# Kernel tuning notes

Hardware: AMD Instinct MI355X
Metric: run time of the kernel (lower is better)

Reference implementation:

```python
import jax, jax.numpy as jnp
import numpy as np

H = 256        # hidden_dim
GD = 16        # genome_dim
GL = 16        # genome_len
L = 2          # n_layers
NH = 4         # n_heads
ED = 256       # embed_dim (of generated network)
CS = 256       # chunk_size (== H so chunk feedback into GRU is well-formed)
TOTAL = 4 * ED * ED + 4 * ED          # 263168
NCH = (TOTAL + CS - 1) // CS          # 1028 sequential GRU steps
B = 16


def setup_inputs() -> dict:
    key = jax.random.key(0)
    ks = iter(jax.random.split(key, 32))
    def p(shape, s=0.02):
        return jax.random.normal(next(ks), shape, jnp.float32) * s
    return dict(
        genome_seq=jax.random.normal(next(ks), (B, GL, GD), jnp.float32),
        embed_W=p((H, GD)), embed_b=jnp.zeros((H,), jnp.float32),
        qkv_W=p((L, 3 * H, H)), qkv_b=jnp.zeros((L, 3 * H), jnp.float32),
        attn_out_W=p((L, H, H)), attn_out_b=jnp.zeros((L, H), jnp.float32),
        ln1_g=jnp.ones((L, H), jnp.float32), ln1_b=jnp.zeros((L, H), jnp.float32),
        ln2_g=jnp.ones((L, H), jnp.float32), ln2_b=jnp.zeros((L, H), jnp.float32),
        ffn_W1=p((L, 4 * H, H)), ffn_b1=jnp.zeros((L, 4 * H), jnp.float32),
        ffn_W2=p((L, H, 4 * H)), ffn_b2=jnp.zeros((L, H), jnp.float32),
        gru_Wih=p((3 * H, H)), gru_Whh=p((3 * H, H)),
        gru_bih=jnp.zeros((3 * H,), jnp.float32), gru_bhh=jnp.zeros((3 * H,), jnp.float32),
        out_W=p((CS, H)), out_b=jnp.zeros((CS,), jnp.float32),
    )


def _ln(x, g, b, eps=1e-5):
    m = x.mean(-1, keepdims=True)
    v = ((x - m) ** 2).mean(-1, keepdims=True)
    return (x - m) / jnp.sqrt(v + eps) * g + b


def reference(genome_seq, embed_W, embed_b, qkv_W, qkv_b, attn_out_W, attn_out_b,
              ln1_g, ln1_b, ln2_g, ln2_b, ffn_W1, ffn_b1, ffn_W2, ffn_b2,
              gru_Wih, gru_Whh, gru_bih, gru_bhh, out_W, out_b):
    b = genome_seq.shape[0]
    dh = H // NH
    scale = 1.0 / np.sqrt(dh).astype(np.float32)

    h = genome_seq @ embed_W.T + embed_b                      # [B, S, H]
    # post-norm transformer encoder, relu FFN (PyTorch defaults, no dropout)
    for l in range(L):
        qkv = h @ qkv_W[l].T + qkv_b[l]                        # [B, S, 3H]
        q, k, v = jnp.split(qkv, 3, axis=-1)
        q = q.reshape(b, GL, NH, dh)
        k = k.reshape(b, GL, NH, dh)
        v = v.reshape(b, GL, NH, dh)
        scores = jnp.einsum('bshd,bthd->bhst', q, k) * scale
        attn = jax.nn.softmax(scores, axis=-1)
        o = jnp.einsum('bhst,bthd->bshd', attn, v).reshape(b, GL, H)
        h = _ln(h + o @ attn_out_W[l].T + attn_out_b[l], ln1_g[l], ln1_b[l])
        f = jax.nn.relu(h @ ffn_W1[l].T + ffn_b1[l]) @ ffn_W2[l].T + ffn_b2[l]
        h = _ln(h + f, ln2_g[l], ln2_b[l])

    latent = h.mean(axis=1)                                    # [B, H]

    # sequential chunk generation: 1 GRU step + Linear per chunk, fed back
    def step(carry, _):
        x, hid = carry
        gi = x @ gru_Wih.T + gru_bih
        gh = hid @ gru_Whh.T + gru_bhh
        ir, iz, inn = jnp.split(gi, 3, axis=-1)
        hr, hz, hn = jnp.split(gh, 3, axis=-1)
        r = jax.nn.sigmoid(ir + hr)
        z = jax.nn.sigmoid(iz + hz)
        n = jnp.tanh(inn + r * hn)
        hid = (1.0 - z) * n + z * hid
        chunk = hid @ out_W.T + out_b                          # [B, CS]
        return (chunk, hid), chunk

    h0 = jnp.zeros((b, H), latent.dtype)
    _, chunks = jax.lax.scan(step, (latent, h0), None, length=NCH)  # [NCH, B, CS]
    flat = jnp.moveaxis(chunks, 0, 1).reshape(b, NCH * CS)
    return flat[:, :TOTAL]
```

## Files before the change

kernel.cpp:

```cpp
#include <hip/hip_runtime.h>


typedef unsigned int uint_t;
typedef int v4i __attribute__((ext_vector_type(4)));

static constexpr size_t WS_HB   = 0;
static constexpr size_t WS_AO   = 262144;
static constexpr size_t WS_GI0  = 593920;
static constexpr size_t WS_CV   = 606208;
static constexpr size_t WS_MS   = 607232;
static constexpr size_t WS_M8   = 608256;
static constexpr size_t WS_HSEQ = 673792;

__device__ inline float sigf(float x){
    return __builtin_amdgcn_rcpf(1.0f + __builtin_amdgcn_exp2f(-1.442695041f*x));
}
__device__ inline float tanh_fast(float x){
    return 1.0f - 2.0f*__builtin_amdgcn_rcpf(1.0f + __builtin_amdgcn_exp2f(2.885390082f*x));
}


__global__ __launch_bounds__(256) void k_emb_prep(
    const float* gs, const float* eW, const float* eb,
    const float* Wih, const float* Whh, const float* bih, const float* bhh,
    const float* outW, const float* outb, float* ws)
{
    __shared__ float wrow[256]; __shared__ float red[256];
    __shared__ signed char q8[256];

    if(blockIdx.x < 256){
        int bs = blockIdx.x;
        int i  = threadIdx.x;
        const float* g = gs + bs*16;
        float acc = eb[i];
#pragma unroll
        for(int d=0; d<16; ++d) acc += g[d]*eW[i*16+d];
        ws[WS_HB + (size_t)bs*256 + i] = acc;
        return;
    }

    int r = blockIdx.x - 256, c = threadIdx.x;
    bool hasA = (r<768);
    wrow[c] = hasA ? Wih[(size_t)r*256+c] : 0.0f;
    __syncthreads();
    float m;
    if(hasA){
        float a=0.f;
        for(int k=0;k<256;++k) a += wrow[k]*outW[(size_t)k*256+c];
        if(r<512) a += Whh[(size_t)r*256+c];
        m=a;
    } else {
        m = Whh[(size_t)(r-256)*256+c];
    }
    red[c] = wrow[c]*outb[c];
    __syncthreads();
    for(int off=128;off>0;off>>=1){ if(c<off) red[c]+=red[c+off]; __syncthreads(); }
    if(c==0){
        float cv;
        if(r<512)       cv = red[0] + bih[r] + bhh[r];
        else if(r<768)  cv = red[0] + bih[r];
        else            cv = bhh[r-256];
        ws[WS_CV + r] = cv;
    }
    __syncthreads();
    red[c] = fabsf(m);
    __syncthreads();
    for(int off=128;off>0;off>>=1){ if(c<off) red[c]=fmaxf(red[c],red[c+off]); __syncthreads(); }
    float rowmax = red[0];
    float inv = rowmax>0.f ? 127.0f/rowmax : 0.0f;
    q8[c] = (signed char)__float2int_rn(m*inv);
    if(c==0) ws[WS_MS + r] = rowmax>0.f ? rowmax*(1.0f/(127.0f*127.0f)) : 0.0f;
    __syncthreads();
    if(c<64){
        uint_t u = ((uint_t)(unsigned char)q8[4*c  ])
                 | ((uint_t)(unsigned char)q8[4*c+1] << 8)
                 | ((uint_t)(unsigned char)q8[4*c+2] << 16)
                 | ((uint_t)(unsigned char)q8[4*c+3] << 24);
        ((uint_t*)ws)[WS_M8 + (size_t)r*64 + c] = u;
    }
}


__global__ __launch_bounds__(256) void k_qkv_attn(const float* qkvW, const float* qkvb,
                                                  float* ws, int l){
    __shared__ float s_h[16][256];
    __shared__ float s_q[16][64], s_k[16][64], s_v[16][64];
    __shared__ float s_sc[16][16];
    int b = blockIdx.x>>2, hh = blockIdx.x&3;
    int tid = threadIdx.x;

    for(int u=tid; u<4096; u+=256)
        s_h[u>>8][u&255] = ws[WS_HB + (size_t)(b*16+(u>>8))*256 + (u&255)];
    __syncthreads();

    if(tid<192){
        int p = tid>>6, d = tid&63;
        int row = l*768 + p*256 + hh*64 + d;
        const float* wr = qkvW + (size_t)row*256;
        float bias = qkvb[row];
        float acc[16];
#pragma unroll
        for(int s=0;s<16;++s) acc[s]=bias;
        for(int k=0;k<256;k+=4){
            float4 w4 = *(const float4*)(wr+k);
#pragma unroll
            for(int s=0;s<16;++s){
                float4 h4 = *(const float4*)&s_h[s][k];
                acc[s] += w4.x*h4.x + w4.y*h4.y + w4.z*h4.z + w4.w*h4.w;
            }
        }
        float (*dst)[64] = (p==0) ? s_q : (p==1) ? s_k : s_v;
#pragma unroll
        for(int s=0;s<16;++s) dst[s][d] = acc[s];
    }
    __syncthreads();

    {
        int s = tid>>4, t = tid&15;
        float a=0.f;
#pragma unroll
        for(int d=0; d<64; ++d) a += s_q[s][d]*s_k[t][d];
        s_sc[s][t] = a*0.125f;
    }
    __syncthreads();
    if(tid<16){
        int r=tid;
        float m=-1e30f;
#pragma unroll
        for(int tt=0;tt<16;++tt) m=fmaxf(m,s_sc[r][tt]);
        float e[16]; float sum=0.f;
#pragma unroll
        for(int tt=0;tt<16;++tt){ e[tt]=__expf(s_sc[r][tt]-m); sum+=e[tt]; }
        float inv=1.0f/sum;
#pragma unroll
        for(int tt=0;tt<16;++tt) s_sc[r][tt]=e[tt]*inv;
    }
    __syncthreads();
    for(int u=tid; u<1024; u+=256){
        int s=u>>6, d=u&63;
        float o=0.f;
#pragma unroll
        for(int t2=0;t2<16;++t2) o += s_sc[s][t2]*s_v[t2][d];
        ws[WS_AO + (size_t)(b*16+s)*256 + hh*64 + d] = o;
    }
}


__global__ __launch_bounds__(256) void k_ao_ffn(
    const float* aoW, const float* aob, const float* g1, const float* b1,
    const float* W1, const float* fb1, const float* W2, const float* fb2,
    const float* g2, const float* b2v, float* ws, int l)
{
    __shared__ float s_x[256];
    __shared__ float s_f1[1024];
    __shared__ float red[256];
    int bs = blockIdx.x, i = threadIdx.x;

    s_x[i] = ws[WS_AO + (size_t)bs*256 + i];
    float hb = ws[WS_HB + (size_t)bs*256 + i];
    __syncthreads();

    const float* wr = aoW + (size_t)(l*256+i)*256;
    float acc = aob[l*256+i];
    for(int k=0;k<256;k+=4){
        float4 w4 = *(const float4*)(wr+k);
        float4 h4 = *(const float4*)&s_x[k];
        acc += w4.x*h4.x + w4.y*h4.y + w4.z*h4.z + w4.w*h4.w;
    }
    float x = hb + acc;
    red[i]=x; __syncthreads();
    for(int off=128;off>0;off>>=1){ if(i<off) red[i]+=red[i+off]; __syncthreads(); }
    float mn = red[0]*(1.0f/256.0f); __syncthreads();
    float d = x-mn;
    red[i]=d*d; __syncthreads();
    for(int off=128;off>0;off>>=1){ if(i<off) red[i]+=red[i+off]; __syncthreads(); }
    float vv = red[0]*(1.0f/256.0f);
    float h1 = (d / sqrtf(vv+1e-5f))*g1[l*256+i] + b1[l*256+i];
    __syncthreads();
    s_x[i] = h1;
    __syncthreads();

#pragma unroll
    for(int jj=0;jj<4;++jj){
        int j = jj*256 + i;
        const float* w1r = W1 + (size_t)(l*1024+j)*256;
        float a1 = fb1[l*1024+j];
        for(int k=0;k<256;k+=4){
            float4 w4 = *(const float4*)(w1r+k);
            float4 h4 = *(const float4*)&s_x[k];
            a1 += w4.x*h4.x + w4.y*h4.y + w4.z*h4.z + w4.w*h4.w;
        }
        s_f1[j] = fmaxf(a1, 0.0f);
    }
    __syncthreads();

    const float* w2r = W2 + (size_t)(l*256+i)*1024;
    float a2 = fb2[l*256+i];
    for(int k=0;k<1024;k+=4){
        float4 w4 = *(const float4*)(w2r+k);
        float4 h4 = *(const float4*)&s_f1[k];
        a2 += w4.x*h4.x + w4.y*h4.y + w4.z*h4.z + w4.w*h4.w;
    }
    float x2 = h1 + a2;
    red[i]=x2; __syncthreads();
    for(int off=128;off>0;off>>=1){ if(i<off) red[i]+=red[i+off]; __syncthreads(); }
    float mn2 = red[0]*(1.0f/256.0f); __syncthreads();
    float d2 = x2-mn2;
    red[i]=d2*d2; __syncthreads();
    for(int off=128;off>0;off>>=1){ if(i<off) red[i]+=red[i+off]; __syncthreads(); }
    float vv2 = red[0]*(1.0f/256.0f);
    float y2 = d2 / sqrtf(vv2+1e-5f);
    ws[WS_HB + (size_t)bs*256 + i] = y2*g2[l*256+i] + b2v[l*256+i];
}


__global__ __launch_bounds__(768) void k_lat_gi0(const float* Wih, const float* bih,
                                                 float* ws){
    __shared__ float lat[256];
    int b=blockIdx.x, j=threadIdx.x;
    if(j<256){
        float a=0.f;
#pragma unroll
        for(int s=0;s<16;++s) a += ws[WS_HB + (size_t)(b*16+s)*256 + j];
        lat[j] = a*(1.0f/16.0f);
    }
    __syncthreads();
    const float* wr = Wih + (size_t)j*256;
    float acc = bih[j];
    for(int k=0;k<256;k+=4){
        float4 w4=*(const float4*)(wr+k);
        float4 l4=*(const float4*)&lat[k];
        acc += w4.x*l4.x + w4.y*l4.y + w4.z*l4.z + w4.w*l4.w;
    }
    ws[WS_GI0 + (size_t)b*768 + j] = acc;
}


__global__ __launch_bounds__(512,2) void k_chain(const float* bhh, float* ws){
    __shared__ alignas(16) signed char h8[2][256];
    int tid = threadIdx.x;
    int b   = blockIdx.x;
    int l   = tid & 63;
    int w   = tid >> 6;
    int col = l & 15;
    int grp = l >> 4;
    int par = grp & 1;
    int ge  = w*32 + par*16 + col;

    const uint_t* Mdw = (const uint_t*)ws + WS_M8;

    v4i wf[8][4];
#pragma unroll
    for(int s=0;s<4;++s){
#pragma unroll
        for(int half=0; half<2; ++half){
            int f = s*2 + half;
            int row = s*256 + w*32 + half*16 + col;
            const uint_t* src = Mdw + (size_t)row*64 + grp*4;
#pragma unroll
            for(int kt=0;kt<4;++kt)
                wf[f][kt] = *(const v4i*)(src + kt*16);
        }
    }
    float Cs[4], MSs[4];
#pragma unroll
    for(int s=0;s<4;++s){
        int row = s*256 + ge;
        Cs[s]  = ws[WS_CV + row];
        MSs[s] = ws[WS_MS + row];
    }

    const float* gi = ws + WS_GI0 + (size_t)b*768;
    float r0 = sigf(gi[ge]     + bhh[ge]);
    float z0 = sigf(gi[256+ge] + bhh[256+ge]);
    float n0 = tanh_fast(gi[512+ge] + r0*bhh[512+ge]);
    float hp = (1.0f-z0)*n0;

    float* hsp = ws + WS_HSEQ + (size_t)b*256;
    if(grp < 2){
        h8[0][w*32 + (l&31)] = (signed char)__float2int_rn(hp*127.0f);
        hsp[w*32 + (l&31)] = hp;
    }
    asm volatile("s_waitcnt lgkmcnt(0)" ::: "memory");
    __builtin_amdgcn_s_barrier();
    asm volatile("" ::: "memory");

    const v4i vzero = {0,0,0,0};
    int po = 0;
    for(int t=1; t<1028; ++t){
        hsp += 4096;
        v4i af[4];
#pragma unroll
        for(int kt=0;kt<4;++kt)
            af[kt] = *(const v4i*)&h8[po][kt*64 + grp*16];
        v4i acc[8];
#pragma unroll
        for(int f=0;f<8;++f){
            acc[f] = __builtin_amdgcn_mfma_i32_16x16x64_i8(af[0], wf[f][0], vzero, 0,0,0);
#pragma unroll
            for(int kt=1;kt<4;++kt)
                acc[f] = __builtin_amdgcn_mfma_i32_16x16x64_i8(af[kt], wf[f][kt], acc[f], 0,0,0);
        }
        int a_r = par ? acc[1][0] : acc[0][0];
        int a_z = par ? acc[3][0] : acc[2][0];
        int a_n = par ? acc[5][0] : acc[4][0];
        int a_h = par ? acc[7][0] : acc[6][0];
        float yr = MSs[0]*(float)a_r + Cs[0];
        float yz = MSs[1]*(float)a_z + Cs[1];
        float yn = MSs[2]*(float)a_n + Cs[2];
        float yh = MSs[3]*(float)a_h + Cs[3];
        float rr = sigf(yr);
        float zz = sigf(yz);
        float nn = tanh_fast(yn + rr*yh);
        hp = (1.0f-zz)*nn + zz*hp;
        if(grp < 2){
            h8[po^1][w*32 + (l&31)] = (signed char)__float2int_rn(hp*127.0f);
            hsp[w*32 + (l&31)] = hp;
        }
        asm volatile("s_waitcnt lgkmcnt(0)" ::: "memory");
        __builtin_amdgcn_s_barrier();
        asm volatile("" ::: "memory");
        po ^= 1;
    }
}

__global__ __launch_bounds__(256) void k_epi(const float* outW, const float* outb,
                                             const float* ws, float* out){
    __shared__ float ht[16][256];
    int t = blockIdx.x, j = threadIdx.x;
    for(int idx=j; idx<4096; idx+=256)
        ht[idx>>8][idx&255] = ws[WS_HSEQ + (size_t)t*4096 + idx];
    __syncthreads();
    const float* wr = outW + (size_t)j*256;
    float bias = outb[j];
    float acc[16];
#pragma unroll
    for(int bb=0;bb<16;++bb) acc[bb]=bias;
    for(int k=0;k<256;k+=4){
        float4 w4 = *(const float4*)(wr+k);
#pragma unroll
        for(int bb=0;bb<16;++bb)
            acc[bb] += w4.x*ht[bb][k]+w4.y*ht[bb][k+1]+w4.z*ht[bb][k+2]+w4.w*ht[bb][k+3];
    }
#pragma unroll
    for(int bb=0;bb<16;++bb)
        out[(size_t)bb*263168 + (size_t)t*256 + j] = acc[bb];
}


extern "C" void kernel_launch(void* const* d_in, const int* in_sizes, int n_in,
                              void* d_out, int out_size, void* d_ws, size_t ws_size,
                              hipStream_t stream){
    const float* gs   = (const float*)d_in[0];
    const float* eW   = (const float*)d_in[1];
    const float* eb   = (const float*)d_in[2];
    const float* qkvW = (const float*)d_in[3];
    const float* qkvb = (const float*)d_in[4];
    const float* aoW  = (const float*)d_in[5];
    const float* aob  = (const float*)d_in[6];
    const float* g1   = (const float*)d_in[7];
    const float* b1   = (const float*)d_in[8];
    const float* g2   = (const float*)d_in[9];
    const float* b2   = (const float*)d_in[10];
    const float* W1   = (const float*)d_in[11];
    const float* fb1  = (const float*)d_in[12];
    const float* W2   = (const float*)d_in[13];
    const float* fb2  = (const float*)d_in[14];
    const float* Wih  = (const float*)d_in[15];
    const float* Whh  = (const float*)d_in[16];
    const float* bih  = (const float*)d_in[17];
    const float* bhh  = (const float*)d_in[18];
    const float* outW = (const float*)d_in[19];
    const float* outb = (const float*)d_in[20];
    float* ws  = (float*)d_ws;
    float* out = (float*)d_out;

    k_emb_prep<<<1280,256,0,stream>>>(gs,eW,eb,Wih,Whh,bih,bhh,outW,outb,ws);
    for(int l=0;l<2;++l){
        k_qkv_attn<<<64,256,0,stream>>>(qkvW,qkvb,ws,l);
        k_ao_ffn  <<<256,256,0,stream>>>(aoW,aob,g1,b1,W1,fb1,W2,fb2,g2,b2,ws,l);
    }
    k_lat_gi0<<<16,768,0,stream>>>(Wih,bih,ws);
    k_chain  <<<16,512,0,stream>>>(bhh,ws);
    k_epi    <<<1028,256,0,stream>>>(outW,outb,ws,out);
}
```

Measured before the change: 1.096 ms.

## Fuse all stages into one cooperative persistent kernel with grid syncs

Replaces the seven separate kernel launches with a single cooperative kernel of 128 blocks that steps through embedding, transformer layers, GRU weight prep, the sequential chain and the epilogue, using grid.sync between stages. The weight-quantization prep now runs on idle blocks in parallel with the layer-0 attention, and its reductions use wave shuffles. This targets launch overhead and inter-kernel gaps. In exchange the epilogue and FFN stages run on only 128 blocks instead of up to 1028, so there is less parallelism and more register pressure from the merged kernel.

```diff
diff --git a/kernel.cpp b/kernel.cpp
--- a/kernel.cpp
+++ b/kernel.cpp
@@ -1,4 +1,7 @@
 #include <hip/hip_runtime.h>
+#include <hip/hip_cooperative_groups.h>
+
+namespace cg = cooperative_groups;
 
 
 typedef unsigned int uint_t;
@@ -19,332 +22,336 @@
     return 1.0f - 2.0f*__builtin_amdgcn_rcpf(1.0f + __builtin_amdgcn_exp2f(2.885390082f*x));
 }
 
-
-__global__ __launch_bounds__(256) void k_emb_prep(
+__global__ __launch_bounds__(512,2) void k_all(
     const float* gs, const float* eW, const float* eb,
-    const float* Wih, const float* Whh, const float* bih, const float* bhh,
-    const float* outW, const float* outb, float* ws)
+    const float* qkvW, const float* qkvb,
+    const float* aoW, const float* aob,
+    const float* g1, const float* b1, const float* g2, const float* b2v,
+    const float* W1, const float* fb1, const float* W2, const float* fb2,
+    const float* Wih, const float* bih, const float* Whh, const float* bhh,
+    const float* outW, const float* outb,
+    float* ws, float* out)
 {
-    __shared__ float wrow[256]; __shared__ float red[256];
-    __shared__ signed char q8[256];
-
-    if(blockIdx.x < 256){
-        int bs = blockIdx.x;
-        int i  = threadIdx.x;
+    __shared__ float s_h[16][256];
+    __shared__ float s_qkv[3][16][64];
+    __shared__ float s_sc[16][16];
+    __shared__ float s_f1[2][1024];
+    __shared__ float s_red[2][256];
+    __shared__ signed char s_h8[2][256];
+
+    cg::grid_group grid = cg::this_grid();
+    int tid = threadIdx.x;
+    int bx  = blockIdx.x;
+
+    {
+        int bs = bx*2 + (tid>>8);
+        int i  = tid & 255;
         const float* g = gs + bs*16;
         float acc = eb[i];
 #pragma unroll
         for(int d=0; d<16; ++d) acc += g[d]*eW[i*16+d];
         ws[WS_HB + (size_t)bs*256 + i] = acc;
-        return;
-    }
-
-    int r = blockIdx.x - 256, c = threadIdx.x;
-    bool hasA = (r<768);
-    wrow[c] = hasA ? Wih[(size_t)r*256+c] : 0.0f;
-    __syncthreads();
-    float m;
-    if(hasA){
-        float a=0.f;
-        for(int k=0;k<256;++k) a += wrow[k]*outW[(size_t)k*256+c];
-        if(r<512) a += Whh[(size_t)r*256+c];
-        m=a;
-    } else {
-        m = Whh[(size_t)(r-256)*256+c];
-    }
-    red[c] = wrow[c]*outb[c];
-    __syncthreads();
-    for(int off=128;off>0;off>>=1){ if(c<off) red[c]+=red[c+off]; __syncthreads(); }
-    if(c==0){
-        float cv;
-        if(r<512)       cv = red[0] + bih[r] + bhh[r];
-        else if(r<768)  cv = red[0] + bih[r];
-        else            cv = bhh[r-256];
-        ws[WS_CV + r] = cv;
-    }
-    __syncthreads();
-    red[c] = fabsf(m);
-    __syncthreads();
-    for(int off=128;off>0;off>>=1){ if(c<off) red[c]=fmaxf(red[c],red[c+off]); __syncthreads(); }
-    float rowmax = red[0];
-    float inv = rowmax>0.f ? 127.0f/rowmax : 0.0f;
-    q8[c] = (signed char)__float2int_rn(m*inv);
-    if(c==0) ws[WS_MS + r] = rowmax>0.f ? rowmax*(1.0f/(127.0f*127.0f)) : 0.0f;
-    __syncthreads();
-    if(c<64){
-        uint_t u = ((uint_t)(unsigned char)q8[4*c  ])
-                 | ((uint_t)(unsigned char)q8[4*c+1] << 8)
-                 | ((uint_t)(unsigned char)q8[4*c+2] << 16)
-                 | ((uint_t)(unsigned char)q8[4*c+3] << 24);
-        ((uint_t*)ws)[WS_M8 + (size_t)r*64 + c] = u;
-    }
-}
-
-
-__global__ __launch_bounds__(256) void k_qkv_attn(const float* qkvW, const float* qkvb,
-                                                  float* ws, int l){
-    __shared__ float s_h[16][256];
-    __shared__ float s_q[16][64], s_k[16][64], s_v[16][64];
-    __shared__ float s_sc[16][16];
-    int b = blockIdx.x>>2, hh = blockIdx.x&3;
-    int tid = threadIdx.x;
-
-    for(int u=tid; u<4096; u+=256)
-        s_h[u>>8][u&255] = ws[WS_HB + (size_t)(b*16+(u>>8))*256 + (u&255)];
-    __syncthreads();
-
-    if(tid<192){
-        int p = tid>>6, d = tid&63;
-        int row = l*768 + p*256 + hh*64 + d;
-        const float* wr = qkvW + (size_t)row*256;
-        float bias = qkvb[row];
-        float acc[16];
-#pragma unroll
-        for(int s=0;s<16;++s) acc[s]=bias;
-        for(int k=0;k<256;k+=4){
-            float4 w4 = *(const float4*)(wr+k);
-#pragma unroll
-            for(int s=0;s<16;++s){
-                float4 h4 = *(const float4*)&s_h[s][k];
-                acc[s] += w4.x*h4.x + w4.y*h4.y + w4.z*h4.z + w4.w*h4.w;
-            }
-        }
-        float (*dst)[64] = (p==0) ? s_q : (p==1) ? s_k : s_v;
-#pragma unroll
-        for(int s=0;s<16;++s) dst[s][d] = acc[s];
-    }
-    __syncthreads();
-
-    {
-        int s = tid>>4, t = tid&15;
-        float a=0.f;
-#pragma unroll
-        for(int d=0; d<64; ++d) a += s_q[s][d]*s_k[t][d];
-        s_sc[s][t] = a*0.125f;
-    }
-    __syncthreads();
-    if(tid<16){
-        int r=tid;
-        float m=-1e30f;
-#pragma unroll
-        for(int tt=0;tt<16;++tt) m=fmaxf(m,s_sc[r][tt]);
-        float e[16]; float sum=0.f;
-#pragma unroll
-        for(int tt=0;tt<16;++tt){ e[tt]=__expf(s_sc[r][tt]-m); sum+=e[tt]; }
-        float inv=1.0f/sum;
-#pragma unroll
-        for(int tt=0;tt<16;++tt) s_sc[r][tt]=e[tt]*inv;
-    }
-    __syncthreads();
-    for(int u=tid; u<1024; u+=256){
-        int s=u>>6, d=u&63;
-        float o=0.f;
-#pragma unroll
-        for(int t2=0;t2<16;++t2) o += s_sc[s][t2]*s_v[t2][d];
-        ws[WS_AO + (size_t)(b*16+s)*256 + hh*64 + d] = o;
-    }
-}
-
-
-__global__ __launch_bounds__(256) void k_ao_ffn(
-    const float* aoW, const float* aob, const float* g1, const float* b1,
-    const float* W1, const float* fb1, const float* W2, const float* fb2,
-    const float* g2, const float* b2v, float* ws, int l)
-{
-    __shared__ float s_x[256];
-    __shared__ float s_f1[1024];
-    __shared__ float red[256];
-    int bs = blockIdx.x, i = threadIdx.x;
-
-    s_x[i] = ws[WS_AO + (size_t)bs*256 + i];
-    float hb = ws[WS_HB + (size_t)bs*256 + i];
-    __syncthreads();
-
-    const float* wr = aoW + (size_t)(l*256+i)*256;
-    float acc = aob[l*256+i];
-    for(int k=0;k<256;k+=4){
-        float4 w4 = *(const float4*)(wr+k);
-        float4 h4 = *(const float4*)&s_x[k];
-        acc += w4.x*h4.x + w4.y*h4.y + w4.z*h4.z + w4.w*h4.w;
-    }
-    float x = hb + acc;
-    red[i]=x; __syncthreads();
-    for(int off=128;off>0;off>>=1){ if(i<off) red[i]+=red[i+off]; __syncthreads(); }
-    float mn = red[0]*(1.0f/256.0f); __syncthreads();
-    float d = x-mn;
-    red[i]=d*d; __syncthreads();
-    for(int off=128;off>0;off>>=1){ if(i<off) red[i]+=red[i+off]; __syncthreads(); }
-    float vv = red[0]*(1.0f/256.0f);
-    float h1 = (d / sqrtf(vv+1e-5f))*g1[l*256+i] + b1[l*256+i];
-    __syncthreads();
-    s_x[i] = h1;
-    __syncthreads();
-
-#pragma unroll
-    for(int jj=0;jj<4;++jj){
-        int j = jj*256 + i;
-        const float* w1r = W1 + (size_t)(l*1024+j)*256;
-        float a1 = fb1[l*1024+j];
-        for(int k=0;k<256;k+=4){
-            float4 w4 = *(const float4*)(w1r+k);
-            float4 h4 = *(const float4*)&s_x[k];
-            a1 += w4.x*h4.x + w4.y*h4.y + w4.z*h4.z + w4.w*h4.w;
-        }
-        s_f1[j] = fmaxf(a1, 0.0f);
-    }
-    __syncthreads();
-
-    const float* w2r = W2 + (size_t)(l*256+i)*1024;
-    float a2 = fb2[l*256+i];
-    for(int k=0;k<1024;k+=4){
-        float4 w4 = *(const float4*)(w2r+k);
-        float4 h4 = *(const float4*)&s_f1[k];
-        a2 += w4.x*h4.x + w4.y*h4.y + w4.z*h4.z + w4.w*h4.w;
-    }
-    float x2 = h1 + a2;
-    red[i]=x2; __syncthreads();
-    for(int off=128;off>0;off>>=1){ if(i<off) red[i]+=red[i+off]; __syncthreads(); }
-    float mn2 = red[0]*(1.0f/256.0f); __syncthreads();
-    float d2 = x2-mn2;
-    red[i]=d2*d2; __syncthreads();
-    for(int off=128;off>0;off>>=1){ if(i<off) red[i]+=red[i+off]; __syncthreads(); }
-    float vv2 = red[0]*(1.0f/256.0f);
-    float y2 = d2 / sqrtf(vv2+1e-5f);
-    ws[WS_HB + (size_t)bs*256 + i] = y2*g2[l*256+i] + b2v[l*256+i];
-}
-
-
-__global__ __launch_bounds__(768) void k_lat_gi0(const float* Wih, const float* bih,
-                                                 float* ws){
-    __shared__ float lat[256];
-    int b=blockIdx.x, j=threadIdx.x;
-    if(j<256){
-        float a=0.f;
-#pragma unroll
-        for(int s=0;s<16;++s) a += ws[WS_HB + (size_t)(b*16+s)*256 + j];
-        lat[j] = a*(1.0f/16.0f);
-    }
-    __syncthreads();
-    const float* wr = Wih + (size_t)j*256;
-    float acc = bih[j];
-    for(int k=0;k<256;k+=4){
-        float4 w4=*(const float4*)(wr+k);
-        float4 l4=*(const float4*)&lat[k];
-        acc += w4.x*l4.x + w4.y*l4.y + w4.z*l4.z + w4.w*l4.w;
-    }
-    ws[WS_GI0 + (size_t)b*768 + j] = acc;
-}
-
-
-__global__ __launch_bounds__(512,2) void k_chain(const float* bhh, float* ws){
-    __shared__ alignas(16) signed char h8[2][256];
-    int tid = threadIdx.x;
-    int b   = blockIdx.x;
-    int l   = tid & 63;
-    int w   = tid >> 6;
-    int col = l & 15;
-    int grp = l >> 4;
-    int par = grp & 1;
-    int ge  = w*32 + par*16 + col;
-
-    const uint_t* Mdw = (const uint_t*)ws + WS_M8;
-
-    v4i wf[8][4];
-#pragma unroll
-    for(int s=0;s<4;++s){
-#pragma unroll
-        for(int half=0; half<2; ++half){
-            int f = s*2 + half;
-            int row = s*256 + w*32 + half*16 + col;
-            const uint_t* src = Mdw + (size_t)row*64 + grp*4;
-#pragma unroll
-            for(int kt=0;kt<4;++kt)
-                wf[f][kt] = *(const v4i*)(src + kt*16);
-        }
-    }
-    float Cs[4], MSs[4];
-#pragma unroll
-    for(int s=0;s<4;++s){
-        int row = s*256 + ge;
-        Cs[s]  = ws[WS_CV + row];
-        MSs[s] = ws[WS_MS + row];
-    }
-
-    const float* gi = ws + WS_GI0 + (size_t)b*768;
-    float r0 = sigf(gi[ge]     + bhh[ge]);
-    float z0 = sigf(gi[256+ge] + bhh[256+ge]);
-    float n0 = tanh_fast(gi[512+ge] + r0*bhh[512+ge]);
-    float hp = (1.0f-z0)*n0;
-
-    float* hsp = ws + WS_HSEQ + (size_t)b*256;
-    if(grp < 2){
-        h8[0][w*32 + (l&31)] = (signed char)__float2int_rn(hp*127.0f);
-        hsp[w*32 + (l&31)] = hp;
-    }
-    asm volatile("s_waitcnt lgkmcnt(0)" ::: "memory");
-    __builtin_amdgcn_s_barrier();
-    asm volatile("" ::: "memory");
-
-    const v4i vzero = {0,0,0,0};
-    int po = 0;
-    for(int t=1; t<1028; ++t){
-        hsp += 4096;
-        v4i af[4];
-#pragma unroll
-        for(int kt=0;kt<4;++kt)
-            af[kt] = *(const v4i*)&h8[po][kt*64 + grp*16];
-        v4i acc[8];
-#pragma unroll
-        for(int f=0;f<8;++f){
-            acc[f] = __builtin_amdgcn_mfma_i32_16x16x64_i8(af[0], wf[f][0], vzero, 0,0,0);
-#pragma unroll
-            for(int kt=1;kt<4;++kt)
-                acc[f] = __builtin_amdgcn_mfma_i32_16x16x64_i8(af[kt], wf[f][kt], acc[f], 0,0,0);
-        }
-        int a_r = par ? acc[1][0] : acc[0][0];
-        int a_z = par ? acc[3][0] : acc[2][0];
-        int a_n = par ? acc[5][0] : acc[4][0];
-        int a_h = par ? acc[7][0] : acc[6][0];
-        float yr = MSs[0]*(float)a_r + Cs[0];
-        float yz = MSs[1]*(float)a_z + Cs[1];
-        float yn = MSs[2]*(float)a_n + Cs[2];
-        float yh = MSs[3]*(float)a_h + Cs[3];
-        float rr = sigf(yr);
-        float zz = sigf(yz);
-        float nn = tanh_fast(yn + rr*yh);
-        hp = (1.0f-zz)*nn + zz*hp;
+    }
+    grid.sync();
+
+    for(int l=0; l<2; ++l){
+        if(bx < 64){
+            int b = bx>>2, hh = bx&3;
+            for(int u=tid; u<4096; u+=512)
+                s_h[u>>8][u&255] = ws[WS_HB + (size_t)(b*16+(u>>8))*256 + (u&255)];
+            __syncthreads();
+            if(tid<192){
+                int p = tid>>6, d = tid&63;
+                int row = l*768 + p*256 + hh*64 + d;
+                const float* wr = qkvW + (size_t)row*256;
+                float bias = qkvb[row];
+                float acc[16];
+#pragma unroll
+                for(int s=0;s<16;++s) acc[s]=bias;
+                for(int k=0;k<256;k+=4){
+                    float4 w4 = *(const float4*)(wr+k);
+#pragma unroll
+                    for(int s=0;s<16;++s){
+                        float4 h4 = *(const float4*)&s_h[s][k];
+                        acc[s] += w4.x*h4.x + w4.y*h4.y + w4.z*h4.z + w4.w*h4.w;
+                    }
+                }
+#pragma unroll
+                for(int s=0;s<16;++s) s_qkv[p][s][d] = acc[s];
+            }
+            __syncthreads();
+            if(tid<256){
+                int s = tid>>4, t = tid&15;
+                float a=0.f;
+#pragma unroll
+                for(int d=0; d<64; ++d) a += s_qkv[0][s][d]*s_qkv[1][t][d];
+                s_sc[s][t] = a*0.125f;
+            }
+            __syncthreads();
+            if(tid<16){
+                int r=tid;
+                float m=-1e30f;
+#pragma unroll
+                for(int tt=0;tt<16;++tt) m=fmaxf(m,s_sc[r][tt]);
+                float e[16]; float sum=0.f;
+#pragma unroll
+                for(int tt=0;tt<16;++tt){ e[tt]=__expf(s_sc[r][tt]-m); sum+=e[tt]; }
+                float inv=1.0f/sum;
+#pragma unroll
+                for(int tt=0;tt<16;++tt) s_sc[r][tt]=e[tt]*inv;
+            }
+            __syncthreads();
+            for(int u=tid; u<1024; u+=512){
+                int s=u>>6, d=u&63;
+                float o=0.f;
+#pragma unroll
+                for(int t2=0;t2<16;++t2) o += s_sc[s][t2]*s_qkv[2][t2][d];
+                ws[WS_AO + (size_t)(b*16+s)*256 + hh*64 + d] = o;
+            }
+        } else if(l==0){
+            int pb = bx - 64;
+            float* wrow = &s_f1[0][0];
+            float* redf = &s_red[0][0];
+            signed char* q8 = (signed char*)&s_sc[0][0];
+            int rh = tid>>8, c = tid&255, wv = tid>>6;
+            for(int it=0; it<8; ++it){
+                int r = pb*16 + it*2 + rh;
+                bool hasA = (r < 768);
+                wrow[rh*256+c] = hasA ? Wih[(size_t)r*256+c] : 0.0f;
+                __syncthreads();
+                float m;
+                if(hasA){
+                    float a = 0.f;
+                    for(int k=0;k<256;++k) a += wrow[rh*256+k]*outW[(size_t)k*256+c];
+                    if(r<512) a += Whh[(size_t)r*256+c];
+                    m = a;
+                } else {
+                    m = Whh[(size_t)(r-256)*256+c];
+                }
+                float pv = wrow[rh*256+c]*outb[c];
+                for(int mk=1; mk<64; mk<<=1) pv += __shfl_xor(pv, mk);
+                if((tid&63)==0) redf[wv] = pv;
+                __syncthreads();
+                if(c==0){
+                    float cs = redf[rh*4+0]+redf[rh*4+1]+redf[rh*4+2]+redf[rh*4+3];
+                    float cv;
+                    if(r<512)       cv = cs + bih[r] + bhh[r];
+                    else if(r<768)  cv = cs + bih[r];
+                    else            cv = bhh[r-256];
+                    ws[WS_CV + r] = cv;
+                }
+                float av = fabsf(m);
+                for(int mk=1; mk<64; mk<<=1) av = fmaxf(av, __shfl_xor(av, mk));
+                if((tid&63)==0) redf[16+wv] = av;
+                __syncthreads();
+                float rowmax = fmaxf(fmaxf(redf[16+rh*4],redf[17+rh*4]),
+                                     fmaxf(redf[18+rh*4],redf[19+rh*4]));
+                float inv = rowmax>0.f ? 127.0f/rowmax : 0.0f;
+                q8[rh*256+c] = (signed char)__float2int_rn(m*inv);
+                if(c==0) ws[WS_MS + r] = rowmax>0.f ? rowmax*(1.0f/(127.0f*127.0f)) : 0.0f;
+                __syncthreads();
+                if(c<64){
+                    uint_t u = ((uint_t)(unsigned char)q8[rh*256+4*c  ])
+                             | ((uint_t)(unsigned char)q8[rh*256+4*c+1] << 8)
+                             | ((uint_t)(unsigned char)q8[rh*256+4*c+2] << 16)
+                             | ((uint_t)(unsigned char)q8[rh*256+4*c+3] << 24);
+                    ((uint_t*)ws)[WS_M8 + (size_t)r*64 + c] = u;
+                }
+                __syncthreads();
+            }
+        }
+        grid.sync();
+
+        {
+            int tk = tid>>8, i = tid&255;
+            int bs = bx*2 + tk;
+            s_h[tk][i] = ws[WS_AO + (size_t)bs*256 + i];
+            float hb = ws[WS_HB + (size_t)bs*256 + i];
+            __syncthreads();
+            const float* wr = aoW + (size_t)(l*256+i)*256;
+            float acc = aob[l*256+i];
+            for(int k=0;k<256;k+=4){
+                float4 w4 = *(const float4*)(wr+k);
+                float4 h4 = *(const float4*)&s_h[tk][k];
+                acc += w4.x*h4.x + w4.y*h4.y + w4.z*h4.z + w4.w*h4.w;
+            }
+            float x = hb + acc;
+            s_red[tk][i]=x; __syncthreads();
+            for(int off=128;off>0;off>>=1){ if(i<off) s_red[tk][i]+=s_red[tk][i+off]; __syncthreads(); }
+            float mn = s_red[tk][0]*(1.0f/256.0f); __syncthreads();
+            float d = x-mn;
+            s_red[tk][i]=d*d; __syncthreads();
+            for(int off=128;off>0;off>>=1){ if(i<off) s_red[tk][i]+=s_red[tk][i+off]; __syncthreads(); }
+            float vv = s_red[tk][0]*(1.0f/256.0f);
+            float h1 = (d / sqrtf(vv+1e-5f))*g1[l*256+i] + b1[l*256+i];
+            __syncthreads();
+            s_h[2+tk][i] = h1;
+            __syncthreads();
+#pragma unroll
+            for(int jj=0;jj<4;++jj){
+                int j = jj*256 + i;
+                const float* w1r = W1 + (size_t)(l*1024+j)*256;
+                float a1 = fb1[l*1024+j];
+                for(int k=0;k<256;k+=4){
+                    float4 w4 = *(const float4*)(w1r+k);
+                    float4 h4 = *(const float4*)&s_h[2+tk][k];
+                    a1 += w4.x*h4.x + w4.y*h4.y + w4.z*h4.z + w4.w*h4.w;
+                }
+                s_f1[tk][j] = fmaxf(a1, 0.0f);
+            }
+            __syncthreads();
+            const float* w2r = W2 + (size_t)(l*256+i)*1024;
+            float a2 = fb2[l*256+i];
+            for(int k=0;k<1024;k+=4){
+                float4 w4 = *(const float4*)(w2r+k);
+                float4 h4 = *(const float4*)&s_f1[tk][k];
+                a2 += w4.x*h4.x + w4.y*h4.y + w4.z*h4.z + w4.w*h4.w;
+            }
+            float x2 = h1 + a2;
+            s_red[tk][i]=x2; __syncthreads();
+            for(int off=128;off>0;off>>=1){ if(i<off) s_red[tk][i]+=s_red[tk][i+off]; __syncthreads(); }
+            float mn2 = s_red[tk][0]*(1.0f/256.0f); __syncthreads();
+            float d2 = x2-mn2;
+            s_red[tk][i]=d2*d2; __syncthreads();
+            for(int off=128;off>0;off>>=1){ if(i<off) s_red[tk][i]+=s_red[tk][i+off]; __syncthreads(); }
+            float vv2 = s_red[tk][0]*(1.0f/256.0f);
+            float y2 = d2 / sqrtf(vv2+1e-5f);
+            ws[WS_HB + (size_t)bs*256 + i] = y2*g2[l*256+i] + b2v[l*256+i];
+        }
+        grid.sync();
+    }
+
+    if(bx < 16){
+        float* lat = &s_sc[0][0];
+        if(tid<256){
+            float a=0.f;
+#pragma unroll
+            for(int s=0;s<16;++s) a += ws[WS_HB + (size_t)(bx*16+s)*256 + tid];
+            lat[tid] = a*(1.0f/16.0f);
+        }
+        __syncthreads();
+        for(int j=tid; j<768; j+=512){
+            const float* wr = Wih + (size_t)j*256;
+            float acc = bih[j];
+            for(int k=0;k<256;k+=4){
+                float4 w4=*(const float4*)(wr+k);
+                float4 l4=*(const float4*)&lat[k];
+                acc += w4.x*l4.x + w4.y*l4.y + w4.z*l4.z + w4.w*l4.w;
+            }
+            ws[WS_GI0 + (size_t)bx*768 + j] = acc;
+        }
+    }
+    grid.sync();
+
+    if(bx < 16){
+        int b   = bx;
+        int ln  = tid & 63;
+        int w   = tid >> 6;
+        int col = ln & 15;
+        int grp = ln >> 4;
+        int par = grp & 1;
+        int ge  = w*32 + par*16 + col;
+
+        const uint_t* Mdw = (const uint_t*)ws + WS_M8;
+        v4i wf[8][4];
+#pragma unroll
+        for(int s=0;s<4;++s){
+#pragma unroll
+            for(int half=0; half<2; ++half){
+                int f = s*2 + half;
+                int row = s*256 + w*32 + half*16 + col;
+                const uint_t* src = Mdw + (size_t)row*64 + grp*4;
+#pragma unroll
+                for(int kt=0;kt<4;++kt)
+                    wf[f][kt] = *(const v4i*)(src + kt*16);
+            }
+        }
+        float Cs[4], MSs[4];
+#pragma unroll
+        for(int s=0;s<4;++s){
+            int row = s*256 + ge;
+            Cs[s]  = ws[WS_CV + row];
+            MSs[s] = ws[WS_MS + row];
+        }
+
+        const float* gi = ws + WS_GI0 + (size_t)b*768;
+        float r0 = sigf(gi[ge]     + bhh[ge]);
+        float z0 = sigf(gi[256+ge] + bhh[256+ge]);
+        float n0 = tanh_fast(gi[512+ge] + r0*bhh[512+ge]);
+        float hp = (1.0f-z0)*n0;
+
+        float* hsp = ws + WS_HSEQ + (size_t)b*256;
         if(grp < 2){
-            h8[po^1][w*32 + (l&31)] = (signed char)__float2int_rn(hp*127.0f);
-            hsp[w*32 + (l&31)] = hp;
+            s_h8[0][w*32 + (ln&31)] = (signed char)__float2int_rn(hp*127.0f);
+            hsp[w*32 + (ln&31)] = hp;
         }
         asm volatile("s_waitcnt lgkmcnt(0)" ::: "memory");
         __builtin_amdgcn_s_barrier();
         asm volatile("" ::: "memory");
-        po ^= 1;
-    }
-}
-
-__global__ __launch_bounds__(256) void k_epi(const float* outW, const float* outb,
-                                             const float* ws, float* out){
-    __shared__ float ht[16][256];
-    int t = blockIdx.x, j = threadIdx.x;
-    for(int idx=j; idx<4096; idx+=256)
-        ht[idx>>8][idx&255] = ws[WS_HSEQ + (size_t)t*4096 + idx];
-    __syncthreads();
-    const float* wr = outW + (size_t)j*256;
-    float bias = outb[j];
-    float acc[16];
-#pragma unroll
-    for(int bb=0;bb<16;++bb) acc[bb]=bias;
-    for(int k=0;k<256;k+=4){
-        float4 w4 = *(const float4*)(wr+k);
-#pragma unroll
-        for(int bb=0;bb<16;++bb)
-            acc[bb] += w4.x*ht[bb][k]+w4.y*ht[bb][k+1]+w4.z*ht[bb][k+2]+w4.w*ht[bb][k+3];
-    }
-#pragma unroll
-    for(int bb=0;bb<16;++bb)
-        out[(size_t)bb*263168 + (size_t)t*256 + j] = acc[bb];
+
+        const v4i vzero = {0,0,0,0};
+        int po = 0;
+        for(int t=1; t<1028; ++t){
+            hsp += 4096;
+            v4i af[4];
+#pragma unroll
+            for(int kt=0;kt<4;++kt)
+                af[kt] = *(const v4i*)&s_h8[po][kt*64 + grp*16];
+            v4i acc[8];
+#pragma unroll
+            for(int f=0;f<8;++f){
+                acc[f] = __builtin_amdgcn_mfma_i32_16x16x64_i8(af[0], wf[f][0], vzero, 0,0,0);
+#pragma unroll
+                for(int kt=1;kt<4;++kt)
+                    acc[f] = __builtin_amdgcn_mfma_i32_16x16x64_i8(af[kt], wf[f][kt], acc[f], 0,0,0);
+            }
+            int a_r = par ? acc[1][0] : acc[0][0];
+            int a_z = par ? acc[3][0] : acc[2][0];
+            int a_n = par ? acc[5][0] : acc[4][0];
+            int a_h = par ? acc[7][0] : acc[6][0];
+            float yr = MSs[0]*(float)a_r + Cs[0];
+            float yz = MSs[1]*(float)a_z + Cs[1];
+            float yn = MSs[2]*(float)a_n + Cs[2];
+            float yh = MSs[3]*(float)a_h + Cs[3];
+            float rr = sigf(yr);
+            float zz = sigf(yz);
+            float nn = tanh_fast(yn + rr*yh);
+            hp = (1.0f-zz)*nn + zz*hp;
+            if(grp < 2){
+                s_h8[po^1][w*32 + (ln&31)] = (signed char)__float2int_rn(hp*127.0f);
+                hsp[w*32 + (ln&31)] = hp;
+            }
+            asm volatile("s_waitcnt lgkmcnt(0)" ::: "memory");
+            __builtin_amdgcn_s_barrier();
+            asm volatile("" ::: "memory");
+            po ^= 1;
+        }
+    }
+    grid.sync();
+
+    for(int t=bx; t<1028; t+=128){
+        for(int u=tid; u<4096; u+=512)
+            (&s_h[0][0])[u] = ws[WS_HSEQ + (size_t)t*4096 + u];
+        __syncthreads();
+        int j = tid & 255, half = tid >> 8;
+        const float* wr = outW + (size_t)j*256;
+        float bias = outb[j];
+        float acc[8];
+#pragma unroll
+        for(int bb=0;bb<8;++bb) acc[bb]=bias;
+        for(int k=0;k<256;k+=4){
+            float4 w4 = *(const float4*)(wr+k);
+#pragma unroll
+            for(int bb=0;bb<8;++bb){
+                float4 h4 = *(const float4*)&s_h[half*8+bb][k];
+                acc[bb] += w4.x*h4.x + w4.y*h4.y + w4.z*h4.z + w4.w*h4.w;
+            }
+        }
+#pragma unroll
+        for(int bb=0;bb<8;++bb)
+            out[(size_t)(half*8+bb)*263168 + (size_t)t*256 + j] = acc[bb];
+        __syncthreads();
+    }
 }
 
 
@@ -375,12 +382,13 @@
     float* ws  = (float*)d_ws;
     float* out = (float*)d_out;
 
-    k_emb_prep<<<1280,256,0,stream>>>(gs,eW,eb,Wih,Whh,bih,bhh,outW,outb,ws);
-    for(int l=0;l<2;++l){
-        k_qkv_attn<<<64,256,0,stream>>>(qkvW,qkvb,ws,l);
-        k_ao_ffn  <<<256,256,0,stream>>>(aoW,aob,g1,b1,W1,fb1,W2,fb2,g2,b2,ws,l);
-    }
-    k_lat_gi0<<<16,768,0,stream>>>(Wih,bih,ws);
-    k_chain  <<<16,512,0,stream>>>(bhh,ws);
-    k_epi    <<<1028,256,0,stream>>>(outW,outb,ws,out);
+    void* args[] = {
+        (void*)&gs, (void*)&eW, (void*)&eb, (void*)&qkvW, (void*)&qkvb,
+        (void*)&aoW, (void*)&aob, (void*)&g1, (void*)&b1, (void*)&g2,
+        (void*)&b2, (void*)&W1, (void*)&fb1, (void*)&W2, (void*)&fb2,
+        (void*)&Wih, (void*)&bih, (void*)&Whh, (void*)&bhh, (void*)&outW,
+        (void*)&outb, (void*)&ws, (void*)&out
+    };
+    hipLaunchCooperativeKernel((const void*)k_all, dim3(128), dim3(512),
+                               args, 0, stream);
 }
```

After: 1.602 ms. 46.2% more time.
